# Kernel tuning notes

Measured on AMD Instinct MI355X. Metric: run time of the kernel, lower is better.

The kernel has to match this reference:

```python
import jax, jax.numpy as jnp
import numpy as np

HEAD_SIZE = 64
INPUT_SIZE = 1024
B, T = 4, 4096


def setup_inputs() -> dict:
    key = jax.random.key(0)
    ks = jax.random.split(key, 7)
    s = 1.0 / np.sqrt(INPUT_SIZE)
    return {
        "x": jax.random.normal(ks[0], (B, T, INPUT_SIZE), dtype=jnp.float32),
        "Wk": jax.random.uniform(ks[1], (INPUT_SIZE, HEAD_SIZE), jnp.float32, -s, s),
        "bk": jax.random.uniform(ks[2], (HEAD_SIZE,), jnp.float32, -s, s),
        "Wq": jax.random.uniform(ks[3], (INPUT_SIZE, HEAD_SIZE), jnp.float32, -s, s),
        "bq": jax.random.uniform(ks[4], (HEAD_SIZE,), jnp.float32, -s, s),
        "Wv": jax.random.uniform(ks[5], (INPUT_SIZE, HEAD_SIZE), jnp.float32, -s, s),
        "bv": jax.random.uniform(ks[6], (HEAD_SIZE,), jnp.float32, -s, s),
    }


def reference(x, Wk, bk, Wq, bq, Wv, bv) -> jnp.ndarray:
    # x: [B, T, D]
    Tlen = x.shape[1]
    k = x @ Wk + bk          # [B, T, H]
    q = x @ Wq + bq          # [B, T, H]
    v = x @ Wv + bv          # [B, T, H]
    scale = 1.0 / jnp.sqrt(jnp.float32(HEAD_SIZE))
    # NOTE: original computes k @ q^T (not q @ k^T) -- keep that exact math.
    w = jnp.einsum("bth,bsh->bts", k, q) * scale  # [B, T, T]
    causal = jnp.tril(jnp.ones((Tlen, Tlen), dtype=bool))
    w = jnp.where(causal, w, -jnp.inf)
    w = jax.nn.softmax(w, axis=-1)
    out = jnp.einsum("bts,bsh->bth", w, v)        # [B, T, H]
    return out
```

## Files before the change

### kernel.cpp

```cpp
#include <hip/hip_runtime.h>
#include <hip/hip_bf16.h>
#include <stdint.h>

typedef __attribute__((ext_vector_type(8))) short short8;
typedef __attribute__((ext_vector_type(4))) float floatx4;

#define HD 64
#define D_IN 1024
#define TLEN 4096
#define NB 4
#define PPB 144
#define LDP 72
#define SL2E 0.18033688011112042f
#define WSZ 196608

__device__ __forceinline__ short f2bf(float f) {
    union { float f; uint32_t u; } v{f};
    uint32_t u = v.u;
    uint32_t r = (u + 0x7FFFu + ((u >> 16) & 1u)) >> 16;
    return (short)r;
}

__device__ __forceinline__ float bf2f(short s) {
    union { uint32_t u; float f; } v;
    v.u = ((uint32_t)(uint16_t)s) << 16;
    return v.f;
}

__device__ __forceinline__ uint32_t pk2(float a, float b) {
    __hip_bfloat162 h = __float22bfloat162_rn(float2{a, b});
    union { __hip_bfloat162 h; uint32_t u; } c{h};
    return c.u;
}

__device__ __forceinline__ void ld_lds16(const void* g, void* l) {
    __builtin_amdgcn_global_load_lds(
        (const __attribute__((address_space(1))) uint32_t*)g,
        (__attribute__((address_space(3))) uint32_t*)l, 16, 0, 0);
}

__global__ __launch_bounds__(256) void prep_w(const float* __restrict__ Wk,
                                              const float* __restrict__ Wq,
                                              const float* __restrict__ Wv,
                                              short* __restrict__ wt) {
    int i = blockIdx.x * 256 + threadIdx.x;
    int j  = i & 7;
    int l  = (i >> 3) & 63;
    int ks = (i >> 9) & 1;
    int rest = i >> 10;
    int f  = rest % 12;
    int kt = rest / 12;
    int mat = f >> 2, nt = f & 3;
    int n = nt * 16 + (l & 15);
    int k = kt * 64 + ks * 32 + (l >> 4) * 8 + j;
    const float* W = (mat == 0) ? Wk : ((mat == 1) ? Wq : Wv);
    wt[i] = f2bf(W[(size_t)k * 64 + n]);
}

__global__ __launch_bounds__(256) void proj(const float* __restrict__ x,
                                            const float* __restrict__ bk,
                                            const float* __restrict__ bq,
                                            const float* __restrict__ bv,
                                            const short* __restrict__ wt,
                                            short* __restrict__ ko,
                                            short* __restrict__ qo,
                                            short* __restrict__ vt) {
    __shared__ float xs[2][2048];

    int tid = threadIdx.x;
    int wave = tid >> 6, lane = tid & 63;
    int quad = lane >> 4, l16 = lane & 15;
    int row0 = blockIdx.x * 32;
    int wbase = tid & ~63;

    floatx4 acc[2][3];
#pragma unroll
    for (int mt = 0; mt < 2; mt++)
#pragma unroll
        for (int fi = 0; fi < 3; fi++) acc[mt][fi] = (floatx4){0.f, 0.f, 0.f, 0.f};

    auto stagex = [&](int kt, int buf) {
#pragma unroll
        for (int it = 0; it < 2; it++) {
            int s = it * 256 + tid;
            int r = s >> 4, p = s & 15;
            int c = (((p >> 1) ^ (r & 7)) << 1) | (p & 1);
            ld_lds16(x + (size_t)(row0 + r) * D_IN + kt * 64 + c * 4,
                     &xs[buf][(it * 256 + wbase) * 4]);
        }
    };

    const short* wv0 = wt + (size_t)(((wave * 3) * 2) * 64 + lane) * 8;

    auto wload = [&](int kt, short8 (&wf)[3][2]) {
#pragma unroll
        for (int fi = 0; fi < 3; fi++)
#pragma unroll
            for (int ks = 0; ks < 2; ks++)
                wf[fi][ks] = *reinterpret_cast<const short8*>(
                    wv0 + (size_t)kt * 12288 + (size_t)((fi * 2 + ks) * 64) * 8);
    };

    auto body = [&](int kt, short8 (&wcur)[3][2], short8 (&wnxt)[3][2]) {
        int buf = kt & 1;
        if (kt < 15) stagex(kt + 1, buf ^ 1);
        __syncthreads();
        if (kt < 15) wload(kt + 1, wnxt);
#pragma unroll
        for (int ks = 0; ks < 2; ks++) {
            short8 av[2];
#pragma unroll
            for (int mt = 0; mt < 2; mt++) {
                int r = mt * 16 + l16;
                int g = ks * 4 + quad;
                const float4* pp = reinterpret_cast<const float4*>(
                    &xs[buf][r * 64 + ((g ^ (r & 7)) << 1) * 4]);
                float4 f0 = pp[0], f1 = pp[1];
                union { uint32_t u[4]; short8 s; } cv;
                cv.u[0] = pk2(f0.x, f0.y); cv.u[1] = pk2(f0.z, f0.w);
                cv.u[2] = pk2(f1.x, f1.y); cv.u[3] = pk2(f1.z, f1.w);
                av[mt] = cv.s;
            }
#pragma unroll
            for (int fi = 0; fi < 3; fi++) {
#pragma unroll
                for (int mt = 0; mt < 2; mt++)
                    acc[mt][fi] = __builtin_amdgcn_mfma_f32_16x16x32_bf16(av[mt], wcur[fi][ks], acc[mt][fi], 0, 0, 0);
            }
        }
        __syncthreads();
    };

    short8 wA[3][2], wB[3][2];
    wload(0, wA);
    stagex(0, 0);
    for (int kt = 0; kt < 16; kt += 2) {
        body(kt, wA, wB);
        body(kt + 1, wB, wA);
    }

#pragma unroll
    for (int fi = 0; fi < 3; fi++) {
        int f = wave * 3 + fi;
        int mat = f >> 2, nt = f & 3;
        int col = nt * 16 + l16;
        const float* bias = (mat == 0) ? bk : ((mat == 1) ? bq : bv);
        float bb = bias[col];
#pragma unroll
        for (int mt = 0; mt < 2; mt++)
#pragma unroll
            for (int reg = 0; reg < 4; reg++) {
                float v = acc[mt][fi][reg] + bb;
                int row = row0 + mt * 16 + quad * 4 + reg;
                if (mat == 0) ko[(size_t)row * HD + col] = f2bf(v * SL2E);
                else if (mat == 1) qo[(size_t)row * HD + col] = f2bf(v);
                else {
                    int bt = row >> 12, tl = row & 4095;
                    vt[(size_t)bt * HD * TLEN + (size_t)col * TLEN + tl] = f2bf(v);
                }
            }
    }
}

template<int SPLIT>
__global__ __launch_bounds__(256) void attn_kern(const short* __restrict__ kb,
                                                 const short* __restrict__ qb,
                                                 const short* __restrict__ vtw,
                                                 short* __restrict__ pO,
                                                 float* __restrict__ pL,
                                                 float* __restrict__ out) {
    __shared__ short Ks[2][4096];
    __shared__ short Vs[2][4096];
    __shared__ short Ps[128 * LDP];

    int tid = threadIdx.x;
    int wave = tid >> 6, lane = tid & 63;
    int quad = lane >> 4, l16 = lane & 15;
    int wbase = tid & ~63;
    int batch = blockIdx.y;

    int tile, j0, j1, slot = 0, nparts = 1;
    if (SPLIT) {
        int bx = blockIdx.x;
        int t = 0, accb = 0;
        for (;;) { int p = (2 * t + 9) >> 3; if (bx < accb + p) break; accb += p; ++t; }
        tile = t;
        j0 = (bx - accb) * 8;
        int je = j0 + 8, lim = 2 * tile + 2;
        j1 = je < lim ? je : lim;
        slot = batch * PPB + bx;
        nparts = (2 * tile + 9) >> 3;
    } else {
        tile = 31 - blockIdx.x;
        j0 = 0; j1 = 2 * tile + 2;
    }
    int t0 = tile * 128;
    int jd = 2 * tile;
    size_t base = (size_t)batch * TLEN * HD;
    const short* vbase = vtw + (size_t)batch * HD * TLEN;

    short8 kf[2][2];
#pragma unroll
    for (int mt = 0; mt < 2; mt++) {
        int trow = t0 + wave * 32 + mt * 16 + l16;
#pragma unroll
        for (int ks = 0; ks < 2; ks++)
            kf[mt][ks] = *reinterpret_cast<const short8*>(kb + base + (size_t)trow * HD + ks * 32 + quad * 8);
    }

    floatx4 o_acc[2][4];
#pragma unroll
    for (int mt = 0; mt < 2; mt++)
#pragma unroll
        for (int ht = 0; ht < 4; ht++) o_acc[mt][ht] = (floatx4){0.f, 0.f, 0.f, 0.f};
    float l_p[2] = {0.f, 0.f};

    auto stage = [&](int j, int buf) {
        int s0 = j * 64;
#pragma unroll
        for (int it = 0; it < 2; it++) {
            int s = it * 256 + tid;
            int r = s >> 3, c = (s & 7) ^ (r & 7);
            ld_lds16(qb + base + (size_t)(s0 + r) * HD + c * 8,
                     &Ks[buf][(it * 256 + wbase) * 8]);
            ld_lds16(vbase + (size_t)r * TLEN + s0 + c * 8,
                     &Vs[buf][(it * 256 + wbase) * 8]);
        }
    };

    stage(j0, 0);
    for (int j = j0; j < j1; ++j) {
        int buf = (j - j0) & 1;
        __syncthreads();
        if (j + 1 < j1) stage(j + 1, buf ^ 1);

        if (j == jd + 1 && wave < 2) continue;

        floatx4 sacc[2][4];
#pragma unroll
        for (int mt = 0; mt < 2; mt++)
#pragma unroll
            for (int nt = 0; nt < 4; nt++) sacc[mt][nt] = (floatx4){0.f, 0.f, 0.f, 0.f};
#pragma unroll
        for (int ks = 0; ks < 2; ks++)
#pragma unroll
            for (int nt = 0; nt < 4; nt++) {
                int r = nt * 16 + l16, g = ks * 4 + quad;
                short8 a = *reinterpret_cast<const short8*>(
                    &Ks[buf][r * 64 + (g ^ (r & 7)) * 8]);
#pragma unroll
                for (int mt = 0; mt < 2; mt++)
                    sacc[mt][nt] = __builtin_amdgcn_mfma_f32_16x16x32_bf16(a, kf[mt][ks], sacc[mt][nt], 0, 0, 0);
            }

        float pv[2][4][4];
#pragma unroll
        for (int mt = 0; mt < 2; mt++)
#pragma unroll
            for (int nt = 0; nt < 4; nt++)
#pragma unroll
                for (int reg = 0; reg < 4; reg++)
                    pv[mt][nt][reg] = __builtin_amdgcn_exp2f(sacc[mt][nt][reg]);
        if (j >= jd) {
            int s0 = j * 64;
#pragma unroll
            for (int mt = 0; mt < 2; mt++) {
                int t_g = t0 + wave * 32 + mt * 16 + l16;
#pragma unroll
                for (int nt = 0; nt < 4; nt++) {
                    int s_g = s0 + nt * 16 + quad * 4;
#pragma unroll
                    for (int reg = 0; reg < 4; reg++)
                        if (s_g + reg > t_g) pv[mt][nt][reg] = 0.f;
                }
            }
        }
#pragma unroll
        for (int mt = 0; mt < 2; mt++) {
            l_p[mt] += ((pv[mt][0][0] + pv[mt][0][1]) + (pv[mt][0][2] + pv[mt][0][3]))
                     + ((pv[mt][1][0] + pv[mt][1][1]) + (pv[mt][1][2] + pv[mt][1][3]))
                     + ((pv[mt][2][0] + pv[mt][2][1]) + (pv[mt][2][2] + pv[mt][2][3]))
                     + ((pv[mt][3][0] + pv[mt][3][1]) + (pv[mt][3][2] + pv[mt][3][3]));
#pragma unroll
            for (int nt = 0; nt < 4; nt++) {
                union { uint32_t u[2]; uint64_t q; } w;
                w.u[0] = pk2(pv[mt][nt][0], pv[mt][nt][1]);
                w.u[1] = pk2(pv[mt][nt][2], pv[mt][nt][3]);
                int row = wave * 32 + mt * 16 + l16;
                *reinterpret_cast<uint64_t*>(&Ps[row * LDP + nt * 16 + quad * 4]) = w.q;
            }
        }

#pragma unroll
        for (int ks = 0; ks < 2; ks++) {
            short8 a[2];
#pragma unroll
            for (int mt = 0; mt < 2; mt++)
                a[mt] = *reinterpret_cast<const short8*>(
                    &Ps[(wave * 32 + mt * 16 + l16) * LDP + ks * 32 + quad * 8]);
#pragma unroll
            for (int ht = 0; ht < 4; ht++) {
                int r = ht * 16 + l16, g = ks * 4 + quad;
                short8 b = *reinterpret_cast<const short8*>(
                    &Vs[buf][r * 64 + (g ^ (r & 7)) * 8]);
#pragma unroll
                for (int mt = 0; mt < 2; mt++)
                    o_acc[mt][ht] = __builtin_amdgcn_mfma_f32_16x16x32_bf16(a[mt], b, o_acc[mt][ht], 0, 0, 0);
            }
        }
    }

#pragma unroll
    for (int mt = 0; mt < 2; mt++) {
        l_p[mt] += __shfl_xor(l_p[mt], 16);
        l_p[mt] += __shfl_xor(l_p[mt], 32);
    }

    if (SPLIT && nparts > 1) {
        short* po = pO + (size_t)slot * 8192;
#pragma unroll
        for (int mt = 0; mt < 2; mt++)
#pragma unroll
            for (int ht = 0; ht < 4; ht++)
#pragma unroll
                for (int reg = 0; reg < 4; reg++) {
                    int lr = wave * 32 + mt * 16 + quad * 4 + reg;
                    po[lr * 64 + ht * 16 + l16] = f2bf(o_acc[mt][ht][reg]);
                }
        if (quad == 0) {
#pragma unroll
            for (int mt = 0; mt < 2; mt++)
                pL[(size_t)slot * 128 + wave * 32 + mt * 16 + l16] = l_p[mt];
        }
    } else {
#pragma unroll
        for (int mt = 0; mt < 2; mt++) {
#pragma unroll
            for (int reg = 0; reg < 4; reg++) {
                float L = __shfl(l_p[mt], quad * 4 + reg, 64);
                float inv = 1.0f / L;
                int t = t0 + wave * 32 + mt * 16 + quad * 4 + reg;
#pragma unroll
                for (int ht = 0; ht < 4; ht++)
                    out[base + (size_t)t * HD + ht * 16 + l16] = o_acc[mt][ht][reg] * inv;
            }
        }
    }
}

__global__ __launch_bounds__(256) void attn_combine(const short* __restrict__ pO,
                                                    const float* __restrict__ pL,
                                                    float* __restrict__ out) {
    int tile = blockIdx.x + 4, batch = blockIdx.y, rq = blockIdx.z;
    int nparts = (2 * tile + 9) >> 3;
    int a = tile >> 2, r = tile & 3;
    int slot0 = batch * PPB + 2 * a * (a + 1) + r * (a + 1);
    int t = threadIdx.x;
    int off = rq * 2048 + t * 8;
    int row = off >> 6;
    int col0 = off & 63;

    float L = 0.f;
    float acc[8];
#pragma unroll
    for (int i = 0; i < 8; i++) acc[i] = 0.f;

    for (int p = 0; p < nparts; ++p) {
        int slot = slot0 + p;
        L += pL[(size_t)slot * 128 + row];
        short8 v = *reinterpret_cast<const short8*>(pO + (size_t)slot * 8192 + off);
#pragma unroll
        for (int i = 0; i < 8; i++) acc[i] += bf2f(v[i]);
    }
    float inv = 1.0f / L;
    float4* dstp = reinterpret_cast<float4*>(out + (size_t)batch * TLEN * HD +
                                             (size_t)(tile * 128 + row) * HD + col0);
#pragma unroll
    for (int c = 0; c < 2; c++) {
        float4 v;
        v.x = acc[c * 4 + 0] * inv; v.y = acc[c * 4 + 1] * inv;
        v.z = acc[c * 4 + 2] * inv; v.w = acc[c * 4 + 3] * inv;
        dstp[c] = v;
    }
}

extern "C" void kernel_launch(void* const* d_in, const int* in_sizes, int n_in,
                              void* d_out, int out_size, void* d_ws, size_t ws_size,
                              hipStream_t stream) {
    const float* x  = (const float*)d_in[0];
    const float* Wk = (const float*)d_in[1];
    const float* bk = (const float*)d_in[2];
    const float* Wq = (const float*)d_in[3];
    const float* bq = (const float*)d_in[4];
    const float* Wv = (const float*)d_in[5];
    const float* bv = (const float*)d_in[6];
    float* out = (float*)d_out;

    const size_t nrow = (size_t)NB * TLEN;
    short* ko = (short*)d_ws;
    short* qo = ko + nrow * HD;
    short* vt = qo + nrow * HD;
    short* wt = vt + nrow * HD;
    short* pO = wt + WSZ;
    float* pL = (float*)(pO + (size_t)NB * PPB * 8192);
    size_t need = (size_t)((char*)(pL + (size_t)NB * PPB * 128) - (char*)d_ws);

    prep_w<<<768, 256, 0, stream>>>(Wk, Wq, Wv, wt);
    proj<<<512, 256, 0, stream>>>(x, bk, bq, bv, wt, ko, qo, vt);
    if (ws_size >= need) {
        attn_kern<1><<<dim3(PPB, NB), 256, 0, stream>>>(ko, qo, vt, pO, pL, out);
        attn_combine<<<dim3(28, NB, 4), 256, 0, stream>>>(pO, pL, out);
    } else {
        attn_kern<0><<<dim3(32, NB), 256, 0, stream>>>(ko, qo, vt, nullptr, nullptr, out);
    }
}
```

Baseline: 149.6 us.

## Load x directly from global into registers in projection, dropping LDS staging

```diff
diff --git a/kernel.cpp b/kernel.cpp
--- a/kernel.cpp
+++ b/kernel.cpp
@@ -65,13 +65,10 @@
                                             short* __restrict__ ko,
                                             short* __restrict__ qo,
                                             short* __restrict__ vt) {
-    __shared__ float xs[2][2048];
-
     int tid = threadIdx.x;
     int wave = tid >> 6, lane = tid & 63;
     int quad = lane >> 4, l16 = lane & 15;
     int row0 = blockIdx.x * 32;
-    int wbase = tid & ~63;
 
     floatx4 acc[2][3];
 #pragma unroll
@@ -79,16 +76,8 @@
 #pragma unroll
         for (int fi = 0; fi < 3; fi++) acc[mt][fi] = (floatx4){0.f, 0.f, 0.f, 0.f};
 
-    auto stagex = [&](int kt, int buf) {
-#pragma unroll
-        for (int it = 0; it < 2; it++) {
-            int s = it * 256 + tid;
-            int r = s >> 4, p = s & 15;
-            int c = (((p >> 1) ^ (r & 7)) << 1) | (p & 1);
-            ld_lds16(x + (size_t)(row0 + r) * D_IN + kt * 64 + c * 4,
-                     &xs[buf][(it * 256 + wbase) * 4]);
-        }
-    };
+    const float* xb0 = x + (size_t)(row0 + l16) * D_IN + quad * 8;
+    const float* xb1 = xb0 + (size_t)16 * D_IN;
 
     const short* wv0 = wt + (size_t)(((wave * 3) * 2) * 64 + lane) * 8;
 
@@ -101,42 +90,36 @@
                     wv0 + (size_t)kt * 12288 + (size_t)((fi * 2 + ks) * 64) * 8);
     };
 
-    auto body = [&](int kt, short8 (&wcur)[3][2], short8 (&wnxt)[3][2]) {
-        int buf = kt & 1;
-        if (kt < 15) stagex(kt + 1, buf ^ 1);
-        __syncthreads();
-        if (kt < 15) wload(kt + 1, wnxt);
+    auto xload = [&](const float* xb, int kt, int ks) -> short8 {
+        const float4* p = reinterpret_cast<const float4*>(xb + kt * 64 + ks * 32);
+        float4 f0 = p[0], f1 = p[1];
+        union { uint32_t u[4]; short8 s; } cv;
+        cv.u[0] = pk2(f0.x, f0.y); cv.u[1] = pk2(f0.z, f0.w);
+        cv.u[2] = pk2(f1.x, f1.y); cv.u[3] = pk2(f1.z, f1.w);
+        return cv.s;
+    };
+
+    auto body = [&](int kt, short8 (&wcur)[3][2]) {
 #pragma unroll
         for (int ks = 0; ks < 2; ks++) {
             short8 av[2];
-#pragma unroll
-            for (int mt = 0; mt < 2; mt++) {
-                int r = mt * 16 + l16;
-                int g = ks * 4 + quad;
-                const float4* pp = reinterpret_cast<const float4*>(
-                    &xs[buf][r * 64 + ((g ^ (r & 7)) << 1) * 4]);
-                float4 f0 = pp[0], f1 = pp[1];
-                union { uint32_t u[4]; short8 s; } cv;
-                cv.u[0] = pk2(f0.x, f0.y); cv.u[1] = pk2(f0.z, f0.w);
-                cv.u[2] = pk2(f1.x, f1.y); cv.u[3] = pk2(f1.z, f1.w);
-                av[mt] = cv.s;
-            }
-#pragma unroll
-            for (int fi = 0; fi < 3; fi++) {
+            av[0] = xload(xb0, kt, ks);
+            av[1] = xload(xb1, kt, ks);
+#pragma unroll
+            for (int fi = 0; fi < 3; fi++)
 #pragma unroll
                 for (int mt = 0; mt < 2; mt++)
                     acc[mt][fi] = __builtin_amdgcn_mfma_f32_16x16x32_bf16(av[mt], wcur[fi][ks], acc[mt][fi], 0, 0, 0);
-            }
-        }
-        __syncthreads();
+        }
     };
 
     short8 wA[3][2], wB[3][2];
     wload(0, wA);
-    stagex(0, 0);
     for (int kt = 0; kt < 16; kt += 2) {
-        body(kt, wA, wB);
-        body(kt + 1, wB, wA);
+        wload(kt + 1, wB);
+        body(kt, wA);
+        if (kt + 2 < 16) wload(kt + 2, wA);
+        body(kt + 1, wB);
     }
 
 #pragma unroll
```

Measured after the change: 165.2 us. +10.4%, slower.

## Deepen projection x staging to four LDS buffers with vmcnt-based waits

Applied to the files above, without the earlier changes.

```diff
diff --git a/kernel.cpp b/kernel.cpp
--- a/kernel.cpp
+++ b/kernel.cpp
@@ -65,7 +65,7 @@
                                             short* __restrict__ ko,
                                             short* __restrict__ qo,
                                             short* __restrict__ vt) {
-    __shared__ float xs[2][2048];
+    __shared__ float xs[4][2048];
 
     int tid = threadIdx.x;
     int wave = tid >> 6, lane = tid & 63;
@@ -79,7 +79,7 @@
 #pragma unroll
         for (int fi = 0; fi < 3; fi++) acc[mt][fi] = (floatx4){0.f, 0.f, 0.f, 0.f};
 
-    auto stagex = [&](int kt, int buf) {
+    auto stage = [&](int kt, int buf) {
 #pragma unroll
         for (int it = 0; it < 2; it++) {
             int s = it * 256 + tid;
@@ -101,11 +101,8 @@
                     wv0 + (size_t)kt * 12288 + (size_t)((fi * 2 + ks) * 64) * 8);
     };
 
-    auto body = [&](int kt, short8 (&wcur)[3][2], short8 (&wnxt)[3][2]) {
-        int buf = kt & 1;
-        if (kt < 15) stagex(kt + 1, buf ^ 1);
-        __syncthreads();
-        if (kt < 15) wload(kt + 1, wnxt);
+    auto body = [&](int kt, short8 (&wcur)[3][2]) {
+        int buf = kt & 3;
 #pragma unroll
         for (int ks = 0; ks < 2; ks++) {
             short8 av[2];
@@ -122,22 +119,36 @@
                 av[mt] = cv.s;
             }
 #pragma unroll
-            for (int fi = 0; fi < 3; fi++) {
+            for (int fi = 0; fi < 3; fi++)
 #pragma unroll
                 for (int mt = 0; mt < 2; mt++)
                     acc[mt][fi] = __builtin_amdgcn_mfma_f32_16x16x32_bf16(av[mt], wcur[fi][ks], acc[mt][fi], 0, 0, 0);
-            }
-        }
-        __syncthreads();
+        }
     };
 
     short8 wA[3][2], wB[3][2];
     wload(0, wA);
-    stagex(0, 0);
-    for (int kt = 0; kt < 16; kt += 2) {
-        body(kt, wA, wB);
-        body(kt + 1, wB, wA);
-    }
+    stage(0, 0); stage(1, 1); stage(2, 2);
+
+    auto step = [&](int kt, short8 (&wcur)[3][2], short8 (&wnxt)[3][2]) {
+        wload(kt + 1, wnxt);
+        asm volatile("s_waitcnt vmcnt(8)" ::: "memory");
+        __builtin_amdgcn_s_barrier();
+        if (kt + 3 < 16) stage(kt + 3, (kt + 3) & 3);
+        body(kt, wcur);
+    };
+
+    for (int kt2 = 0; kt2 < 14; kt2 += 2) {
+        step(kt2, wA, wB);
+        step(kt2 + 1, wB, wA);
+    }
+    wload(15, wB);
+    asm volatile("s_waitcnt vmcnt(6)" ::: "memory");
+    __builtin_amdgcn_s_barrier();
+    body(14, wA);
+    asm volatile("s_waitcnt vmcnt(0)" ::: "memory");
+    __builtin_amdgcn_s_barrier();
+    body(15, wB);
 
 #pragma unroll
     for (int fi = 0; fi < 3; fi++) {
```

After: 149.8 us (median of 2 runs). About the same (+0.1%).

## Restructure projection kernel with 3-stage LDS pipeline and shared weight staging

Applied to the files above, without the earlier changes.

```diff
diff --git a/kernel.cpp b/kernel.cpp
--- a/kernel.cpp
+++ b/kernel.cpp
@@ -13,6 +13,7 @@
 #define LDP 72
 #define SL2E 0.18033688011112042f
 #define WSZ 196608
+#define PROJ_LDS (3 * 40960)
 
 __device__ __forceinline__ short f2bf(float f) {
     union { float f; uint32_t u; } v{f};
@@ -57,7 +58,7 @@
     wt[i] = f2bf(W[(size_t)k * 64 + n]);
 }
 
-__global__ __launch_bounds__(256) void proj(const float* __restrict__ x,
+__global__ __launch_bounds__(512) void proj(const float* __restrict__ x,
                                             const float* __restrict__ bk,
                                             const float* __restrict__ bq,
                                             const float* __restrict__ bv,
@@ -65,100 +66,97 @@
                                             short* __restrict__ ko,
                                             short* __restrict__ qo,
                                             short* __restrict__ vt) {
-    __shared__ float xs[2][2048];
+    extern __shared__ char smem[];
 
     int tid = threadIdx.x;
     int wave = tid >> 6, lane = tid & 63;
     int quad = lane >> 4, l16 = lane & 15;
-    int row0 = blockIdx.x * 32;
     int wbase = tid & ~63;
-
-    floatx4 acc[2][3];
-#pragma unroll
-    for (int mt = 0; mt < 2; mt++)
-#pragma unroll
-        for (int fi = 0; fi < 3; fi++) acc[mt][fi] = (floatx4){0.f, 0.f, 0.f, 0.f};
-
-    auto stagex = [&](int kt, int buf) {
+    int row0 = blockIdx.x * 64;
+    int rt = wave >> 1, fg = wave & 1;
+
+    floatx4 acc[6];
+#pragma unroll
+    for (int fi = 0; fi < 6; fi++) acc[fi] = (floatx4){0.f, 0.f, 0.f, 0.f};
+
+    auto xs = [&](int s) -> float* { return (float*)(smem + s * 40960); };
+    auto wsp = [&](int s) -> short* { return (short*)(smem + s * 40960 + 16384); };
+
+    auto stage = [&](int kt, int slot) {
+        float* xd = xs(slot);
+        short* wd = wsp(slot);
 #pragma unroll
         for (int it = 0; it < 2; it++) {
-            int s = it * 256 + tid;
+            int s = it * 512 + tid;
             int r = s >> 4, p = s & 15;
             int c = (((p >> 1) ^ (r & 7)) << 1) | (p & 1);
             ld_lds16(x + (size_t)(row0 + r) * D_IN + kt * 64 + c * 4,
-                     &xs[buf][(it * 256 + wbase) * 4]);
+                     xd + (it * 512 + wbase) * 4);
+        }
+#pragma unroll
+        for (int it = 0; it < 3; it++) {
+            int s = it * 512 + tid;
+            ld_lds16(wt + (size_t)kt * 12288 + (size_t)s * 8,
+                     wd + (it * 512 + wbase) * 8);
         }
     };
 
-    const short* wv0 = wt + (size_t)(((wave * 3) * 2) * 64 + lane) * 8;
-
-    auto wload = [&](int kt, short8 (&wf)[3][2]) {
-#pragma unroll
-        for (int fi = 0; fi < 3; fi++)
-#pragma unroll
-            for (int ks = 0; ks < 2; ks++)
-                wf[fi][ks] = *reinterpret_cast<const short8*>(
-                    wv0 + (size_t)kt * 12288 + (size_t)((fi * 2 + ks) * 64) * 8);
+    auto body = [&](int kt, int slot) {
+        const float* xd = xs(slot);
+        const short* wd = wsp(slot);
+#pragma unroll
+        for (int ks = 0; ks < 2; ks++) {
+            int r = rt * 16 + l16;
+            int g = ks * 4 + quad;
+            const float4* pp = reinterpret_cast<const float4*>(
+                xd + r * 64 + ((g ^ (r & 7)) << 1) * 4);
+            float4 f0 = pp[0], f1 = pp[1];
+            union { uint32_t u[4]; short8 s; } cv;
+            cv.u[0] = pk2(f0.x, f0.y); cv.u[1] = pk2(f0.z, f0.w);
+            cv.u[2] = pk2(f1.x, f1.y); cv.u[3] = pk2(f1.z, f1.w);
+            short8 av = cv.s;
+#pragma unroll
+            for (int fi = 0; fi < 6; fi++) {
+                int f = fg * 6 + fi;
+                short8 bf = *reinterpret_cast<const short8*>(
+                    wd + ((f * 2 + ks) * 64 + lane) * 8);
+                acc[fi] = __builtin_amdgcn_mfma_f32_16x16x32_bf16(av, bf, acc[fi], 0, 0, 0);
+            }
+        }
     };
 
-    auto body = [&](int kt, short8 (&wcur)[3][2], short8 (&wnxt)[3][2]) {
-        int buf = kt & 1;
-        if (kt < 15) stagex(kt + 1, buf ^ 1);
-        __syncthreads();
-        if (kt < 15) wload(kt + 1, wnxt);
-#pragma unroll
-        for (int ks = 0; ks < 2; ks++) {
-            short8 av[2];
-#pragma unroll
-            for (int mt = 0; mt < 2; mt++) {
-                int r = mt * 16 + l16;
-                int g = ks * 4 + quad;
-                const float4* pp = reinterpret_cast<const float4*>(
-                    &xs[buf][r * 64 + ((g ^ (r & 7)) << 1) * 4]);
-                float4 f0 = pp[0], f1 = pp[1];
-                union { uint32_t u[4]; short8 s; } cv;
-                cv.u[0] = pk2(f0.x, f0.y); cv.u[1] = pk2(f0.z, f0.w);
-                cv.u[2] = pk2(f1.x, f1.y); cv.u[3] = pk2(f1.z, f1.w);
-                av[mt] = cv.s;
-            }
-#pragma unroll
-            for (int fi = 0; fi < 3; fi++) {
-#pragma unroll
-                for (int mt = 0; mt < 2; mt++)
-                    acc[mt][fi] = __builtin_amdgcn_mfma_f32_16x16x32_bf16(av[mt], wcur[fi][ks], acc[mt][fi], 0, 0, 0);
-            }
-        }
-        __syncthreads();
-    };
-
-    short8 wA[3][2], wB[3][2];
-    wload(0, wA);
-    stagex(0, 0);
-    for (int kt = 0; kt < 16; kt += 2) {
-        body(kt, wA, wB);
-        body(kt + 1, wB, wA);
-    }
-
-#pragma unroll
-    for (int fi = 0; fi < 3; fi++) {
-        int f = wave * 3 + fi;
+    stage(0, 0);
+    stage(1, 1);
+    int slot = 0, nslot = 2;
+    for (int kt = 0; kt < 16; kt++) {
+        if (kt < 15) asm volatile("s_waitcnt vmcnt(5)" ::: "memory");
+        else         asm volatile("s_waitcnt vmcnt(0)" ::: "memory");
+        __builtin_amdgcn_s_barrier();
+        __builtin_amdgcn_sched_barrier(0);
+        if (kt + 2 < 16) stage(kt + 2, nslot);
+        body(kt, slot);
+        slot = (slot == 2) ? 0 : slot + 1;
+        nslot = (nslot == 2) ? 0 : nslot + 1;
+    }
+
+#pragma unroll
+    for (int fi = 0; fi < 6; fi++) {
+        int f = fg * 6 + fi;
         int mat = f >> 2, nt = f & 3;
         int col = nt * 16 + l16;
         const float* bias = (mat == 0) ? bk : ((mat == 1) ? bq : bv);
         float bb = bias[col];
 #pragma unroll
-        for (int mt = 0; mt < 2; mt++)
-#pragma unroll
-            for (int reg = 0; reg < 4; reg++) {
-                float v = acc[mt][fi][reg] + bb;
-                int row = row0 + mt * 16 + quad * 4 + reg;
-                if (mat == 0) ko[(size_t)row * HD + col] = f2bf(v * SL2E);
-                else if (mat == 1) qo[(size_t)row * HD + col] = f2bf(v);
-                else {
-                    int bt = row >> 12, tl = row & 4095;
-                    vt[(size_t)bt * HD * TLEN + (size_t)col * TLEN + tl] = f2bf(v);
-                }
-            }
+        for (int reg = 0; reg < 4; reg++) {
+            float v = acc[fi][reg] + bb;
+            int row = row0 + rt * 16 + quad * 4 + reg;
+            if (mat == 0) ko[(size_t)row * HD + col] = f2bf(v * SL2E);
+            else if (mat == 1) qo[(size_t)row * HD + col] = f2bf(v);
+            else {
+                int bt = row >> 12, tl = row & 4095;
+                vt[(size_t)bt * HD * TLEN + (size_t)col * TLEN + tl] = f2bf(v);
+            }
+        }
     }
 }
 
@@ -405,8 +403,16 @@
     float* pL = (float*)(pO + (size_t)NB * PPB * 8192);
     size_t need = (size_t)((char*)(pL + (size_t)NB * PPB * 128) - (char*)d_ws);
 
+    static int attr_set = 0;
+    if (!attr_set) {
+        (void)hipFuncSetAttribute((const void*)proj,
+                                  hipFuncAttributeMaxDynamicSharedMemorySize,
+                                  PROJ_LDS);
+        attr_set = 1;
+    }
+
     prep_w<<<768, 256, 0, stream>>>(Wk, Wq, Wv, wt);
-    proj<<<512, 256, 0, stream>>>(x, bk, bq, bv, wt, ko, qo, vt);
+    proj<<<256, 512, PROJ_LDS, stream>>>(x, bk, bq, bv, wt, ko, qo, vt);
     if (ws_size >= need) {
         attn_kern<1><<<dim3(PPB, NB), 256, 0, stream>>>(ko, qo, vt, pO, pL, out);
         attn_combine<<<dim3(28, NB, 4), 256, 0, stream>>>(pO, pL, out);
```

Result: no change. 152.4 us (+1.9%).
